# Optimization experiments

Measured on AMD Instinct MI355X. Metric: run time of the kernel, lower is better.

## Reference

```python
import jax, jax.numpy as jnp
import numpy as np

ATOM_VOC = 128
APO = 128
NHEAD = 16
D_MODEL = 512
BOND_VOC = 32
CHIRAL_VOC = 4
B, L = 4, 384


def setup_inputs() -> dict:
    key = jax.random.key(0)
    ks = jax.random.split(key, 12)
    atoms = jax.random.randint(ks[0], (B, L), 0, ATOM_VOC)
    chirals = jax.random.randint(ks[1], (B, L), 0, CHIRAL_VOC)
    coordinates = jax.random.normal(ks[2], (B, L, 3), dtype=jnp.float32)
    bonds = jax.random.randint(ks[3], (B, L, L), 0, BOND_VOC)
    # embedding tables; padding_idx rows (0) zeroed to match torch padding_idx
    atype_emb = jax.random.normal(ks[4], (ATOM_VOC, D_MODEL), dtype=jnp.float32) * 0.02
    atype_emb = atype_emb.at[0].set(0.0)
    chiral_emb = jax.random.normal(ks[5], (CHIRAL_VOC, D_MODEL), dtype=jnp.float32) * 0.02
    chiral_emb = chiral_emb.at[0].set(0.0)
    apair_w_emb = jax.random.normal(ks[6], (ATOM_VOC * ATOM_VOC, APO), dtype=jnp.float32) * 0.02
    apair_b_emb = jax.random.normal(ks[7], (ATOM_VOC * ATOM_VOC, APO), dtype=jnp.float32) * 0.02
    means = jax.random.normal(ks[8], (APO,), dtype=jnp.float32) * 0.1
    stds = jnp.ones((APO,), dtype=jnp.float32) + jax.random.normal(ks[9], (APO,), dtype=jnp.float32) * 0.1
    bond_emb = jax.random.normal(ks[10], (BOND_VOC, NHEAD), dtype=jnp.float32) * 0.02
    bond_emb = bond_emb.at[0].set(0.0)
    lin_w = jax.random.normal(ks[11], (NHEAD, APO), dtype=jnp.float32) * (1.0 / np.sqrt(APO))
    lin_b = jnp.zeros((NHEAD,), dtype=jnp.float32)
    return dict(atoms=atoms, chirals=chirals, coordinates=coordinates, bonds=bonds,
                atype_emb=atype_emb, chiral_emb=chiral_emb,
                apair_w_emb=apair_w_emb, apair_b_emb=apair_b_emb,
                means=means, stds=stds, bond_emb=bond_emb, lin_w=lin_w, lin_b=lin_b)


def reference(atoms, chirals, coordinates, bonds, atype_emb, chiral_emb,
              apair_w_emb, apair_b_emb, means, stds, bond_emb, lin_w, lin_b):
    # atoms: [b,l] int; coordinates: [b,l,3]; bonds: [b,l,l] int
    atoms_emb = atype_emb[atoms] + chiral_emb[chirals]          # [b,l,d]
    atoms_emb = jnp.transpose(atoms_emb, (1, 0, 2))             # [l,b,d]
    diff = coordinates[:, None, :, :] - coordinates[:, :, None, :]  # [b,l,l,3]
    d2 = jnp.sum(diff * diff, axis=-1)
    distances = jnp.sqrt(d2 + 1e-12)                            # [b,l,l] (eps avoids nan grad on diag)
    apair_idx = atoms[:, None, :] * ATOM_VOC + atoms[:, :, None]  # [b,l,l]
    ap = apair_w_emb[apair_idx] * distances[..., None] + apair_b_emb[apair_idx]  # [b,l,l,apo]
    s = jnp.abs(stds) + 1e-5
    ap = jnp.exp(-0.5 * jnp.square((ap - means) / s)) / (np.sqrt(2 * np.pi) * s)
    ap = jnp.einsum('bijk,hk->bijh', ap, lin_w) + lin_b + bond_emb[bonds]  # [b,l,l,nhead]
    pad = (atoms == 0)[:, None, :, None]                        # mask key atoms (dim 2)
    ap = jnp.where(pad, -jnp.inf, ap)
    ap = jnp.transpose(ap, (0, 3, 1, 2))                        # [b,nhead,l,l]
    return atoms_emb, ap
```

## Files before the change

kernel.cpp:

```cpp
#include <hip/hip_runtime.h>
#include <hip/hip_fp16.h>
#include <math.h>
#include <string.h>

#define ATOM_VOC 128
#define APO      128
#define NHEAD    16
#define D_MODEL  512
#define NB       4
#define NL       384

typedef __attribute__((ext_vector_type(8))) _Float16 f16x8;
typedef __attribute__((ext_vector_type(4))) float    f32x4;
typedef __attribute__((ext_vector_type(4))) unsigned u32x4;

#define PACK_DWORDS (ATOM_VOC * ATOM_VOC * APO)
#define BFT_SHORTS  (4 * 4 * 16 * 8)

static __device__ inline unsigned short f2h(float x) {
    __half h = __float2half(x);
    unsigned short u; memcpy(&u, &h, 2); return u;
}

static __device__ inline void gload_lds16(const void* g, void* l) {
    __builtin_amdgcn_global_load_lds(
        (const __attribute__((address_space(1))) void*)g,
        (__attribute__((address_space(3))) void*)l, 16, 0, 0);
}

__global__ __launch_bounds__(256) void pack_kernel(
    const float* __restrict__ apw, const float* __restrict__ apb,
    const float* __restrict__ means, const float* __restrict__ stds,
    const float* __restrict__ lin_w,
    unsigned* __restrict__ pack, unsigned short* __restrict__ bft, int write_bft)
{
    const int t     = threadIdx.x;
    const int r     = t >> 5;
    const int u     = t & 31;
    const int ph    = u >> 4;
    const int half  = (u >> 3) & 1;
    const int q     = u & 7;
    const int rowid = blockIdx.x * 8 + r;
    const int ai    = rowid >> 7;
    const int v     = rowid & 127;
    const int kb    = ph * 64 + q * 8;

    const size_t srcrow = ((size_t)v * ATOM_VOC + ai) * APO;
    const float* sp = (half ? apb : apw) + srcrow + kb;
    const float4 f0  = *(const float4*)(sp);
    const float4 f1  = *(const float4*)(sp + 4);
    const float4 sd0 = *(const float4*)(stds + kb);
    const float4 sd1 = *(const float4*)(stds + kb + 4);

    float x[8]  = {f0.x, f0.y, f0.z, f0.w, f1.x, f1.y, f1.z, f1.w};
    float ss[8] = {sd0.x, sd0.y, sd0.z, sd0.w, sd1.x, sd1.y, sd1.z, sd1.w};
    if (half) {
        const float4 m0 = *(const float4*)(means + kb);
        const float4 m1 = *(const float4*)(means + kb + 4);
        const float mm[8] = {m0.x, m0.y, m0.z, m0.w, m1.x, m1.y, m1.z, m1.w};
#pragma unroll
        for (int j = 0; j < 8; ++j) x[j] = x[j] - mm[j];
    }
    unsigned dw[4];
#pragma unroll
    for (int j = 0; j < 4; ++j) {
        const float ag0 = 0.84932180028802f / (fabsf(ss[2 * j])     + 1e-5f);
        const float ag1 = 0.84932180028802f / (fabsf(ss[2 * j + 1]) + 1e-5f);
        dw[j] = ((unsigned)f2h(x[2 * j + 1] * ag1) << 16) | f2h(x[2 * j] * ag0);
    }
    const int dst = ph * 64 + half * 32 + q * 4;
    *(u32x4*)&pack[((size_t)ai * ATOM_VOC + v) * APO + dst] = *(const u32x4*)dw;

    if (write_bft && blockIdx.x == 0) {
        const int cid  = t;
        const int ks   = cid >> 6;
        const int quad = (cid >> 4) & 3;
        const int hh   = cid & 15;
        const int kb2  = ks * 32 + quad * 8;
        unsigned short tmp[8];
#pragma unroll
        for (int uu = 0; uu < 8; ++uu) {
            const int kk = kb2 + uu;
            float z = 0.3989422804014327f / (fabsf(stds[kk]) + 1e-5f);
            tmp[uu] = f2h(lin_w[hh * APO + kk] * z);
        }
        memcpy(&bft[(size_t)cid * 8], tmp, 16);
    }
}

__global__ __launch_bounds__(512, 4) void ap_kernel(
    const int*            __restrict__ atoms,
    const int*            __restrict__ chirals,
    const float*          __restrict__ coords,
    const int*            __restrict__ bonds,
    const unsigned*       __restrict__ pack,
    const unsigned short* __restrict__ bft,
    const float*          __restrict__ atype_emb,
    const float*          __restrict__ chiral_emb,
    const float*          __restrict__ bond_emb,
    const float*          __restrict__ lin_b,
    float*                __restrict__ out1,
    float*                __restrict__ out2)
{
    const int i    = blockIdx.x;
    const int b    = blockIdx.y;
    const int t    = threadIdx.x;
    const int lane = t & 63;
    const int wave = t >> 6;
    const int h    = lane & 15;
    const int quad = lane >> 4;

    __shared__ unsigned tbl[2][ATOM_VOC * 64];

    const int ai = atoms[b * NL + i];
    const unsigned* src = pack + (size_t)ai * (ATOM_VOC * APO);

#pragma unroll
    for (int ph = 0; ph < 2; ++ph) {
#pragma unroll
        for (int itx = 0; itx < 4; ++itx) {
            const int c   = itx * 512 + t;
            const int row = c >> 4;
            const int cc  = c & 15;
            gload_lds16(src + ((size_t)row * 32 + ph * 16 + (cc ^ (row & 15))) * 4,
                        &tbl[ph][(itx * 512 + wave * 64) * 4]);
        }
    }

    {
        const int ch = chirals[b * NL + i];
        out1[((size_t)i * NB + b) * D_MODEL + t] =
            atype_emb[(size_t)ai * D_MODEL + t] +
            chiral_emb[(size_t)ch * D_MODEL + t];
    }

    f16x8 bfrag[4];
#pragma unroll
    for (int ks = 0; ks < 4; ++ks)
        memcpy(&bfrag[ks], bft + ((size_t)((ks * 4 + quad) * 16 + h)) * 8, 16);
    const float lbh = lin_b[h];

    const float cix = coords[((size_t)b * NL + i) * 3 + 0];
    const float ciy = coords[((size_t)b * NL + i) * 3 + 1];
    const float ciz = coords[((size_t)b * NL + i) * 3 + 2];

    int     jv[3];
    __half2 jd2[3];
#pragma unroll
    for (int it = 0; it < 3; ++it) {
        const int j = it * 128 + wave * 16 + h;
        jv[it] = atoms[b * NL + j];
        const float dx = coords[((size_t)b * NL + j) * 3 + 0] - cix;
        const float dy = coords[((size_t)b * NL + j) * 3 + 1] - ciy;
        const float dz = coords[((size_t)b * NL + j) * 3 + 2] - ciz;
        jd2[it] = __half2half2(__float2half(
            sqrtf(fmaf(dx, dx, fmaf(dy, dy, dz * dz)) + 1e-12f)));
    }

    f32x4 acc[3] = {{0.f,0.f,0.f,0.f},{0.f,0.f,0.f,0.f},{0.f,0.f,0.f,0.f}};

    __syncthreads();

#pragma unroll
    for (int ph = 0; ph < 2; ++ph) {
#pragma unroll
        for (int it = 0; it < 3; ++it) {
            const int v  = jv[it];
            const int vb = v * 64;
            const int vx = v & 15;
            const __half2 d2 = jd2[it];
#pragma unroll
            for (int ks2 = 0; ks2 < 2; ++ks2) {
                const u32x4 wch = *(const u32x4*)&tbl[ph][vb + 4 * ((ks2 * 4 + quad) ^ vx)];
                const u32x4 bch = *(const u32x4*)&tbl[ph][vb + 4 * ((8 + ks2 * 4 + quad) ^ vx)];
                unsigned afw[4];
#pragma unroll
                for (int q = 0; q < 4; ++q) {
                    __half2 w2, b2;
                    unsigned wd = wch[q], bd = bch[q];
                    memcpy(&w2, &wd, 4); memcpy(&b2, &bd, 4);
                    __half2 u2  = __hfma2(w2, d2, b2);
                    __half2 nm2 = __hmul2(u2, __hneg2(u2));
                    __half2 g2  = h2exp2(nm2);
                    memcpy(&afw[q], &g2, 4);
                }
                f16x8 af;
                memcpy(&af, afw, 16);
                acc[it] = __builtin_amdgcn_mfma_f32_16x16x32_f16(
                    af, bfrag[ph * 2 + ks2], acc[it], 0, 0, 0);
            }
        }
    }

    const size_t bondrow = ((size_t)b * NL + i) * NL;
    float* op = out2 + (((size_t)(b * NHEAD + h)) * NL + i) * NL;
#pragma unroll
    for (int it = 0; it < 3; ++it) {
        const int jb = it * 128 + wave * 16 + quad * 4;
        const int4 bd = *(const int4*)(bonds + bondrow + jb);
        const int4 aj = *(const int4*)(atoms + b * NL + jb);
        float4 vv;
        vv.x = acc[it][0] + lbh + bond_emb[bd.x * NHEAD + h];
        vv.y = acc[it][1] + lbh + bond_emb[bd.y * NHEAD + h];
        vv.z = acc[it][2] + lbh + bond_emb[bd.z * NHEAD + h];
        vv.w = acc[it][3] + lbh + bond_emb[bd.w * NHEAD + h];
        if (aj.x == 0) vv.x = -1.0e30f;
        if (aj.y == 0) vv.y = -1.0e30f;
        if (aj.z == 0) vv.z = -1.0e30f;
        if (aj.w == 0) vv.w = -1.0e30f;
        *(float4*)(op + jb) = vv;
    }
}

extern "C" void kernel_launch(void* const* d_in, const int* in_sizes, int n_in,
                              void* d_out, int out_size, void* d_ws, size_t ws_size,
                              hipStream_t stream)
{
    const int*   atoms      = (const int*)d_in[0];
    const int*   chirals    = (const int*)d_in[1];
    const float* coords     = (const float*)d_in[2];
    const int*   bonds      = (const int*)d_in[3];
    const float* atype_emb  = (const float*)d_in[4];
    const float* chiral_emb = (const float*)d_in[5];
    const float* apw        = (const float*)d_in[6];
    const float* apb        = (const float*)d_in[7];
    const float* means      = (const float*)d_in[8];
    const float* stds       = (const float*)d_in[9];
    const float* bond_emb   = (const float*)d_in[10];
    const float* lin_w      = (const float*)d_in[11];
    const float* lin_b      = (const float*)d_in[12];
    float* out = (float*)d_out;

    unsigned* pack = (unsigned*)d_ws;
    unsigned short* bftp = (unsigned short*)((char*)d_ws + (size_t)PACK_DWORDS * 4);

    pack_kernel<<<dim3((ATOM_VOC * ATOM_VOC) / 8), dim3(256), 0, stream>>>(
        apw, apb, means, stds, lin_w, pack, bftp, 1);

    {
        float* out2 = out + (size_t)NL * NB * D_MODEL;
        ap_kernel<<<dim3(NL, NB), dim3(512), 0, stream>>>(
            atoms, chirals, coords, bonds, pack, bftp,
            atype_emb, chiral_emb, bond_emb, lin_b, out, out2);
    }
}
```

Baseline: 128.7 us.

## Overlap second-half table load with first-half MFMA compute via split waits

Splits the per-row LDS table fill into two halves. It issues the second half's async global-to-LDS loads after the other prologue loads, then waits with vmcnt(4) so compute on the first half can start while the second half is still in flight. The bond and atom-mask loads for the epilogue are hoisted before the compute loop so their latency is hidden too. This adds hand-counted vmcnt waits and scheduling barriers, which are fragile if the compiler changes the load count or order.

```diff
diff --git a/kernel.cpp b/kernel.cpp
--- a/kernel.cpp
+++ b/kernel.cpp
@@ -116,16 +116,14 @@
     const unsigned* src = pack + (size_t)ai * (ATOM_VOC * APO);
 
 #pragma unroll
-    for (int ph = 0; ph < 2; ++ph) {
-#pragma unroll
-        for (int itx = 0; itx < 4; ++itx) {
-            const int c   = itx * 512 + t;
-            const int row = c >> 4;
-            const int cc  = c & 15;
-            gload_lds16(src + ((size_t)row * 32 + ph * 16 + (cc ^ (row & 15))) * 4,
-                        &tbl[ph][(itx * 512 + wave * 64) * 4]);
-        }
-    }
+    for (int itx = 0; itx < 4; ++itx) {
+        const int c   = itx * 512 + t;
+        const int row = c >> 4;
+        const int cc  = c & 15;
+        gload_lds16(src + ((size_t)row * 32 + (cc ^ (row & 15))) * 4,
+                    &tbl[0][(itx * 512 + wave * 64) * 4]);
+    }
+    __builtin_amdgcn_sched_barrier(0);
 
     {
         const int ch = chirals[b * NL + i];
@@ -157,12 +155,40 @@
             sqrtf(fmaf(dx, dx, fmaf(dy, dy, dz * dz)) + 1e-12f)));
     }
 
+    const size_t bondrow = ((size_t)b * NL + i) * NL;
+    int4 bd4[3], aj4[3];
+#pragma unroll
+    for (int it = 0; it < 3; ++it) {
+        const int jb = it * 128 + wave * 16 + quad * 4;
+        bd4[it] = *(const int4*)(bonds + bondrow + jb);
+        aj4[it] = *(const int4*)(atoms + b * NL + jb);
+    }
+
     f32x4 acc[3] = {{0.f,0.f,0.f,0.f},{0.f,0.f,0.f,0.f},{0.f,0.f,0.f,0.f}};
 
-    __syncthreads();
+    __builtin_amdgcn_sched_barrier(0);
+#pragma unroll
+    for (int itx = 0; itx < 4; ++itx) {
+        const int c   = itx * 512 + t;
+        const int row = c >> 4;
+        const int cc  = c & 15;
+        gload_lds16(src + ((size_t)row * 32 + 16 + (cc ^ (row & 15))) * 4,
+                    &tbl[1][(itx * 512 + wave * 64) * 4]);
+    }
+    __builtin_amdgcn_sched_barrier(0);
+
+    asm volatile("s_waitcnt vmcnt(4)" ::: "memory");
+    __builtin_amdgcn_s_barrier();
+    __builtin_amdgcn_sched_barrier(0);
 
 #pragma unroll
     for (int ph = 0; ph < 2; ++ph) {
+        if (ph) {
+            __builtin_amdgcn_sched_barrier(0);
+            asm volatile("s_waitcnt vmcnt(0)" ::: "memory");
+            __builtin_amdgcn_s_barrier();
+            __builtin_amdgcn_sched_barrier(0);
+        }
 #pragma unroll
         for (int it = 0; it < 3; ++it) {
             const int v  = jv[it];
@@ -192,22 +218,19 @@
         }
     }
 
-    const size_t bondrow = ((size_t)b * NL + i) * NL;
     float* op = out2 + (((size_t)(b * NHEAD + h)) * NL + i) * NL;
 #pragma unroll
     for (int it = 0; it < 3; ++it) {
         const int jb = it * 128 + wave * 16 + quad * 4;
-        const int4 bd = *(const int4*)(bonds + bondrow + jb);
-        const int4 aj = *(const int4*)(atoms + b * NL + jb);
         float4 vv;
-        vv.x = acc[it][0] + lbh + bond_emb[bd.x * NHEAD + h];
-        vv.y = acc[it][1] + lbh + bond_emb[bd.y * NHEAD + h];
-        vv.z = acc[it][2] + lbh + bond_emb[bd.z * NHEAD + h];
-        vv.w = acc[it][3] + lbh + bond_emb[bd.w * NHEAD + h];
-        if (aj.x == 0) vv.x = -1.0e30f;
-        if (aj.y == 0) vv.y = -1.0e30f;
-        if (aj.z == 0) vv.z = -1.0e30f;
-        if (aj.w == 0) vv.w = -1.0e30f;
+        vv.x = acc[it][0] + lbh + bond_emb[bd4[it].x * NHEAD + h];
+        vv.y = acc[it][1] + lbh + bond_emb[bd4[it].y * NHEAD + h];
+        vv.z = acc[it][2] + lbh + bond_emb[bd4[it].z * NHEAD + h];
+        vv.w = acc[it][3] + lbh + bond_emb[bd4[it].w * NHEAD + h];
+        if (aj4[it].x == 0) vv.x = -1.0e30f;
+        if (aj4[it].y == 0) vv.y = -1.0e30f;
+        if (aj4[it].z == 0) vv.z = -1.0e30f;
+        if (aj4[it].w == 0) vv.w = -1.0e30f;
         *(float4*)(op + jb) = vv;
     }
 }
```

New measurement: 127.6 us. About the same (-0.8%).
